# Kernel optimization log

Measured on AMD Instinct MI355X. Metric: run time of the kernel, lower is better.

The kernel has to match this reference:

```python
import jax, jax.numpy as jnp
import numpy as np
from math import sqrt

B, L, S, H, E, D = 2, 2048, 2048, 16, 64, 64

def setup_inputs() -> dict:
    key = jax.random.key(0)
    kq, kk, kv = jax.random.split(key, 3)
    queries = jax.random.normal(kq, (B, L, H, E), dtype=jnp.float32)
    keys = jax.random.normal(kk, (B, S, H, E), dtype=jnp.float32)
    values = jax.random.normal(kv, (B, S, H, D), dtype=jnp.float32)
    # causal mask: True where attention is NOT allowed (j > i), matching masked_fill_ semantics
    causal = jnp.triu(jnp.ones((L, S), dtype=jnp.bool_), k=1)
    attn_mask = jnp.broadcast_to(causal[None, None, :, :], (B, 1, L, S))
    return {"queries": queries, "keys": keys, "values": values, "attn_mask": attn_mask}

def reference(queries, keys, values, attn_mask):
    # scores: [B,H,L,S]
    scale = 1.0 / sqrt(queries.shape[-1])
    scores = jnp.einsum('blhe,bshe->bhls', queries, keys)
    scores = jnp.where(attn_mask, -jnp.inf, scores)
    A = jax.nn.softmax(scale * scores, axis=-1)
    V = jnp.einsum('bhls,bshd->blhd', A, values)
    return V
```

## Files before the change

kernel.cpp:

```cpp
#include <hip/hip_runtime.h>

typedef unsigned short ushort_t;
typedef __attribute__((ext_vector_type(8))) short s8v;
typedef __attribute__((ext_vector_type(2))) unsigned u2v;
typedef __attribute__((ext_vector_type(4))) float f4;

__device__ __forceinline__ ushort_t f2bf(float x) {
    unsigned u = __builtin_bit_cast(unsigned, x);
    return (ushort_t)((u + 0x7FFFu + ((u >> 16) & 1u)) >> 16);
}
__device__ __forceinline__ unsigned pack_hi16(float lo, float hi) {
    unsigned a = __builtin_bit_cast(unsigned, lo);
    unsigned b = __builtin_bit_cast(unsigned, hi);
    return (a >> 16) | (b & 0xFFFF0000u);
}

__global__ __launch_bounds__(256) void prep_kv(const float* __restrict__ K,
                                               const float* __restrict__ V,
                                               ushort_t* __restrict__ Kb,
                                               ushort_t* __restrict__ VT) {
    __shared__ ushort_t T[64 * 72];
    if (blockIdx.x < 2048) {
        const int gid = blockIdx.x * 256 + threadIdx.x;
        const int e = (gid & 7) * 8;
        const int h = (gid >> 3) & 15;
        const int s = (gid >> 7) & 2047;
        const int b = gid >> 18;
        const float* src = K + (((b * 2048 + s) * 16 + h) * 64 + e);
        f4 a = *(const f4*)src;
        f4 c = *(const f4*)(src + 4);
        s8v o;
        #pragma unroll
        for (int j = 0; j < 4; ++j) { o[j] = (short)f2bf(a[j]); o[j + 4] = (short)f2bf(c[j]); }
        *(s8v*)(Kb + (((b * 16 + h) * 2048 + s) * 64 + e)) = o;
    } else {
        const int v = blockIdx.x - 2048;
        const int s0 = (v & 31) * 64;
        const int h  = (v >> 5) & 15;
        const int b  = v >> 9;
        const int t  = threadIdx.x;
        {
            const int srow = t >> 2, dc = (t & 3) * 16;
            const float* src = V + (((b * 2048 + s0 + srow) * 16 + h) * 64 + dc);
            #pragma unroll
            for (int c = 0; c < 4; ++c) {
                f4 vv = *(const f4*)(src + c * 4);
                #pragma unroll
                for (int j = 0; j < 4; ++j) T[(dc + c * 4 + j) * 72 + srow] = f2bf(vv[j]);
            }
        }
        __syncthreads();
        {
            const int d = t >> 2, sq = (t & 3) * 16;
            ushort_t* dst = VT + (((b * 16 + h) * 64 + d) * 2048 + s0 + sq);
            *(s8v*)(dst)     = *(const s8v*)(&T[d * 72 + sq]);
            *(s8v*)(dst + 8) = *(const s8v*)(&T[d * 72 + sq + 8]);
        }
    }
}

__global__ __launch_bounds__(256, 2) void fattn_main(
    const float* __restrict__ Q,
    const ushort_t* __restrict__ Kb,
    const ushort_t* __restrict__ VTb,
    float* __restrict__ O)
{
    constexpr float K1 = 0.18033688011112042f;
    constexpr float SHIFT = 12.0f;
    __shared__ ushort_t KT [64 * 72];
    __shared__ ushort_t VTl[64 * 72];
    __shared__ ushort_t P  [4][16 * 72];

    const int bx = blockIdx.x;
    const int bh = bx & 31;
    const int p  = bx >> 5;
    const int b = bh >> 4, h = bh & 15;

    const int wave = threadIdx.x >> 6;
    const int lane = threadIdx.x & 63;
    const int l15  = lane & 15;
    const int quad = lane >> 4;

    const ushort_t* kb  = Kb  + bh * (2048 * 64);
    const ushort_t* vtb = VTb + bh * (64 * 2048);
    const float*    qb  = Q + b * (2048 * 1024) + h * 64;
    float*          ob  = O + b * (2048 * 1024) + h * 64;

    const s8v ones = {0x3F80, 0x3F80, 0x3F80, 0x3F80, 0x3F80, 0x3F80, 0x3F80, 0x3F80};
    const f4 zero4 = {0.f, 0.f, 0.f, 0.f};

    const int sr = threadIdx.x >> 2;
    const int sc = (threadIdx.x & 3) << 4;

    int qr0 = p * 64;

    s8v aq[2];
    f4 oacc[4];
    f4 lsum;

    auto loadQ = [&](int qr) {
        const float* qrow = qb + (qr + wave * 16 + l15) * 1024;
        #pragma unroll
        for (int ks = 0; ks < 2; ++ks) {
            f4 x = *(const f4*)(qrow + ks * 32 + quad * 8);
            f4 y = *(const f4*)(qrow + ks * 32 + quad * 8 + 4);
            #pragma unroll
            for (int j = 0; j < 4; ++j) {
                aq[ks][j]     = (short)f2bf(x[j]);
                aq[ks][j + 4] = (short)f2bf(y[j]);
            }
        }
    };
    auto zeroAcc = [&]() {
        lsum = zero4;
        #pragma unroll
        for (int d = 0; d < 4; ++d) oacc[d] = zero4;
    };
    auto storeO = [&](int qr) {
        #pragma unroll
        for (int r = 0; r < 4; ++r) {
            const float inv = 1.0f / lsum[r];
            const int row = qr + wave * 16 + quad * 4 + r;
            #pragma unroll
            for (int dd = 0; dd < 4; ++dd)
                ob[row * 1024 + dd * 16 + l15] = oacc[dd][r] * inv;
        }
    };

    loadQ(qr0);
    zeroAcc();

    s8v gK[2], gV[2];
    {
        const ushort_t* ksrc = kb + sr * 64 + sc;
        const ushort_t* vsrc = vtb + sr * 2048 + sc;
        gK[0] = *(const s8v*)(ksrc);     gK[1] = *(const s8v*)(ksrc + 8);
        gV[0] = *(const s8v*)(vsrc);     gV[1] = *(const s8v*)(vsrc + 8);
    }

    for (int n = 0; n < 33; ++n) {
        *(s8v*)&KT [sr * 72 + sc]     = gK[0];
        *(s8v*)&KT [sr * 72 + sc + 8] = gK[1];
        *(s8v*)&VTl[sr * 72 + sc]     = gV[0];
        *(s8v*)&VTl[sr * 72 + sc + 8] = gV[1];
        __syncthreads();

        s8v gK2[2], gV2[2];
        if (n < 32) {
            const int sn = (n + 1 <= p) ? (n + 1) : (n - p);
            const ushort_t* ksrc = kb + (sn * 64 + sr) * 64 + sc;
            const ushort_t* vsrc = vtb + sr * 2048 + sn * 64 + sc;
            gK2[0] = *(const s8v*)(ksrc);    gK2[1] = *(const s8v*)(ksrc + 8);
            gV2[0] = *(const s8v*)(vsrc);    gV2[1] = *(const s8v*)(vsrc + 8);
        }

        const int s_cur = (n <= p) ? n : (n - p - 1);
        const int n0 = s_cur * 64;
        const bool diag = (n == p) || (n == 32);

        f4 st[4];
        #pragma unroll
        for (int t = 0; t < 4; ++t) {
            const s8v bk0 = *(const s8v*)&KT[(t * 16 + l15) * 72 + quad * 8];
            const s8v bk1 = *(const s8v*)&KT[(t * 16 + l15) * 72 + 32 + quad * 8];
            f4 a = __builtin_amdgcn_mfma_f32_16x16x32_bf16(bk0, aq[0], zero4, 0, 0, 0);
            st[t] = __builtin_amdgcn_mfma_f32_16x16x32_bf16(bk1, aq[1], a, 0, 0, 0);
        }

        ushort_t* Pm = P[wave];
        #pragma unroll
        for (int t = 0; t < 4; ++t) {
            float pv[4];
            #pragma unroll
            for (int r = 0; r < 4; ++r) {
                float x = __builtin_fmaf(st[t][r], K1, -SHIFT);
                if (diag) {
                    const int gj = n0 + t * 16 + quad * 4 + r;
                    const int gi = qr0 + wave * 16 + l15;
                    if (gj > gi) x = -INFINITY;
                }
                pv[r] = __builtin_exp2f(x);
            }
            u2v pk;
            pk[0] = pack_hi16(pv[0], pv[1]);
            pk[1] = pack_hi16(pv[2], pv[3]);
            *(u2v*)&Pm[l15 * 72 + t * 16 + quad * 4] = pk;
        }

        #pragma unroll
        for (int ks = 0; ks < 2; ++ks) {
            s8v bvv[4];
            #pragma unroll
            for (int dd = 0; dd < 4; ++dd)
                bvv[dd] = *(const s8v*)&VTl[(dd * 16 + l15) * 72 + ks * 32 + quad * 8];
            const s8v ap = *(const s8v*)&Pm[l15 * 72 + ks * 32 + quad * 8];
            lsum = __builtin_amdgcn_mfma_f32_16x16x32_bf16(ap, ones, lsum, 0, 0, 0);
            #pragma unroll
            for (int dd = 0; dd < 4; ++dd)
                oacc[dd] = __builtin_amdgcn_mfma_f32_16x16x32_bf16(ap, bvv[dd], oacc[dd], 0, 0, 0);
        }

        __syncthreads();

        if (n < 32) {
            gK[0] = gK2[0]; gK[1] = gK2[1];
            gV[0] = gV2[0]; gV[1] = gV2[1];
        }

        if (n == p) {
            storeO(qr0);
            qr0 = (31 - p) * 64;
            loadQ(qr0);
            zeroAcc();
        }
    }

    storeO(qr0);
}

#define PSTR 72
__global__ __launch_bounds__(256) void fattn_fallback(
    const float* __restrict__ Q, const float* __restrict__ K,
    const float* __restrict__ V, float* __restrict__ O)
{
    constexpr int strL = 1024, strB = 2048 * strL;
    const float scale = 0.125f;
    __shared__ ushort_t KT[64 * PSTR];
    __shared__ ushort_t VT[64 * PSTR];
    __shared__ ushort_t P[4][16 * PSTR];
    const int bh = blockIdx.x & 31;
    const int b = bh >> 4, h = bh & 15;
    const int im = 31 - (blockIdx.x >> 5);
    const int q0 = im * 64;
    const int tid = threadIdx.x, wave = tid >> 6, lane = tid & 63;
    const int l15 = lane & 15, quad = lane >> 4;
    const float* qbase = Q + b*strB + (q0 + wave*16 + l15)*strL + h*64;
    s8v aq0, aq1;
    {
        f4 q0v = *(const f4*)(qbase + quad*8);
        f4 q1v = *(const f4*)(qbase + quad*8 + 4);
        f4 q2v = *(const f4*)(qbase + 32 + quad*8);
        f4 q3v = *(const f4*)(qbase + 32 + quad*8 + 4);
        #pragma unroll
        for (int j = 0; j < 4; ++j) {
            aq0[j] = (short)f2bf(q0v[j]); aq0[j+4] = (short)f2bf(q1v[j]);
            aq1[j] = (short)f2bf(q2v[j]); aq1[j+4] = (short)f2bf(q3v[j]);
        }
    }
    const f4 zero4 = {0.f,0.f,0.f,0.f};
    f4 oacc[4]; float m_prev[4], lsum[4];
    #pragma unroll
    for (int d = 0; d < 4; ++d) oacc[d] = zero4;
    #pragma unroll
    for (int r = 0; r < 4; ++r) { m_prev[r] = -INFINITY; lsum[r] = 0.0f; }
    const float* kh = K + b*strB + h*64;
    const float* vh = V + b*strB + h*64;
    for (int it = 0; it <= im; ++it) {
        const int n0 = it * 64;
        __syncthreads();
        {
            const float* krow = kh + (n0 + lane)*strL + wave*16;
            f4 k0 = *(const f4*)(krow); f4 k1 = *(const f4*)(krow+4);
            f4 k2 = *(const f4*)(krow+8); f4 k3 = *(const f4*)(krow+12);
            s8v kb0, kb1;
            #pragma unroll
            for (int j = 0; j < 4; ++j) {
                kb0[j] = (short)f2bf(k0[j]); kb0[j+4] = (short)f2bf(k1[j]);
                kb1[j] = (short)f2bf(k2[j]); kb1[j+4] = (short)f2bf(k3[j]);
            }
            *(s8v*)&KT[lane*PSTR + wave*16] = kb0;
            *(s8v*)&KT[lane*PSTR + wave*16 + 8] = kb1;
            const float* vrow = vh + (n0 + lane)*strL + wave*16;
            f4 v0 = *(const f4*)(vrow); f4 v1 = *(const f4*)(vrow+4);
            f4 v2 = *(const f4*)(vrow+8); f4 v3 = *(const f4*)(vrow+12);
            #pragma unroll
            for (int j = 0; j < 4; ++j) {
                VT[(wave*16 + j)*PSTR + lane] = f2bf(v0[j]);
                VT[(wave*16 + 4 + j)*PSTR + lane] = f2bf(v1[j]);
                VT[(wave*16 + 8 + j)*PSTR + lane] = f2bf(v2[j]);
                VT[(wave*16 + 12 + j)*PSTR + lane] = f2bf(v3[j]);
            }
        }
        __syncthreads();
        f4 sacc[4];
        #pragma unroll
        for (int t = 0; t < 4; ++t) {
            sacc[t] = zero4;
            const s8v bk0 = *(const s8v*)&KT[(t*16 + l15)*PSTR + quad*8];
            const s8v bk1 = *(const s8v*)&KT[(t*16 + l15)*PSTR + 32 + quad*8];
            sacc[t] = __builtin_amdgcn_mfma_f32_16x16x32_bf16(aq0, bk0, sacc[t], 0, 0, 0);
            sacc[t] = __builtin_amdgcn_mfma_f32_16x16x32_bf16(aq1, bk1, sacc[t], 0, 0, 0);
        }
        const bool diag = (it == im);
        float sv[4][4], rmax[4];
        #pragma unroll
        for (int r = 0; r < 4; ++r) rmax[r] = -INFINITY;
        #pragma unroll
        for (int t = 0; t < 4; ++t)
            #pragma unroll
            for (int r = 0; r < 4; ++r) {
                float x = sacc[t][r] * scale;
                if (diag) {
                    const int gi = wave*16 + quad*4 + r;
                    const int gj = t*16 + l15;
                    if (gj > gi) x = -INFINITY;
                }
                sv[t][r] = x; rmax[r] = fmaxf(rmax[r], x);
            }
        #pragma unroll
        for (int off = 8; off >= 1; off >>= 1)
            #pragma unroll
            for (int r = 0; r < 4; ++r)
                rmax[r] = fmaxf(rmax[r], __shfl_xor(rmax[r], off, 64));
        float mnew[4], alpha[4], rsum[4];
        #pragma unroll
        for (int r = 0; r < 4; ++r) {
            mnew[r] = fmaxf(m_prev[r], rmax[r]);
            alpha[r] = __expf(m_prev[r] - mnew[r]);
            m_prev[r] = mnew[r]; rsum[r] = 0.f;
        }
        #pragma unroll
        for (int t = 0; t < 4; ++t)
            #pragma unroll
            for (int r = 0; r < 4; ++r) {
                const float p = __expf(sv[t][r] - mnew[r]);
                rsum[r] += p;
                P[wave][(quad*4 + r)*PSTR + t*16 + l15] = f2bf(p);
            }
        #pragma unroll
        for (int off = 8; off >= 1; off >>= 1)
            #pragma unroll
            for (int r = 0; r < 4; ++r)
                rsum[r] += __shfl_xor(rsum[r], off, 64);
        #pragma unroll
        for (int r = 0; r < 4; ++r) lsum[r] = alpha[r]*lsum[r] + rsum[r];
        #pragma unroll
        for (int d = 0; d < 4; ++d)
            #pragma unroll
            for (int r = 0; r < 4; ++r) oacc[d][r] *= alpha[r];
        #pragma unroll
        for (int ks = 0; ks < 2; ++ks) {
            const s8v ap = *(const s8v*)&P[wave][l15*PSTR + ks*32 + quad*8];
            #pragma unroll
            for (int d = 0; d < 4; ++d) {
                const s8v bvv = *(const s8v*)&VT[(d*16 + l15)*PSTR + ks*32 + quad*8];
                oacc[d] = __builtin_amdgcn_mfma_f32_16x16x32_bf16(ap, bvv, oacc[d], 0, 0, 0);
            }
        }
    }
    float* obase = O + b*strB + h*64;
    #pragma unroll
    for (int r = 0; r < 4; ++r) {
        const float inv = 1.0f / lsum[r];
        const int gi = q0 + wave*16 + quad*4 + r;
        #pragma unroll
        for (int d = 0; d < 4; ++d)
            obase[gi*strL + d*16 + l15] = oacc[d][r] * inv;
    }
}

extern "C" void kernel_launch(void* const* d_in, const int* in_sizes, int n_in,
                              void* d_out, int out_size, void* d_ws, size_t ws_size,
                              hipStream_t stream) {
    const float* Q = (const float*)d_in[0];
    const float* K = (const float*)d_in[1];
    const float* V = (const float*)d_in[2];
    float* O = (float*)d_out;
    const size_t NEED = 2ull * 4194304ull * 2ull;
    if (ws_size >= NEED) {
        ushort_t* Kb = (ushort_t*)d_ws;
        ushort_t* VT = Kb + 4194304;
        prep_kv<<<3072, 256, 0, stream>>>(K, V, Kb, VT);
        fattn_main<<<512, 256, 0, stream>>>(Q, Kb, VT, O);
    } else {
        fattn_fallback<<<1024, 256, 0, stream>>>(Q, K, V, O);
    }
}
```

Baseline: 151.8 us.

## Double-buffer K/V tiles in LDS and raise wave priority around MFMA blocks

```diff
diff --git a/kernel.cpp b/kernel.cpp
--- a/kernel.cpp
+++ b/kernel.cpp
@@ -67,8 +67,10 @@
 {
     constexpr float K1 = 0.18033688011112042f;
     constexpr float SHIFT = 12.0f;
-    __shared__ ushort_t KT [64 * 72];
-    __shared__ ushort_t VTl[64 * 72];
+    __shared__ ushort_t KT0[64 * 72];
+    __shared__ ushort_t KT1[64 * 72];
+    __shared__ ushort_t VT0[64 * 72];
+    __shared__ ushort_t VT1[64 * 72];
     __shared__ ushort_t P  [4][16 * 72];
 
     const int bx = blockIdx.x;
@@ -130,21 +132,24 @@
     loadQ(qr0);
     zeroAcc();
 
-    s8v gK[2], gV[2];
     {
         const ushort_t* ksrc = kb + sr * 64 + sc;
         const ushort_t* vsrc = vtb + sr * 2048 + sc;
-        gK[0] = *(const s8v*)(ksrc);     gK[1] = *(const s8v*)(ksrc + 8);
-        gV[0] = *(const s8v*)(vsrc);     gV[1] = *(const s8v*)(vsrc + 8);
-    }
+        s8v k0 = *(const s8v*)(ksrc);
+        s8v k1 = *(const s8v*)(ksrc + 8);
+        s8v v0 = *(const s8v*)(vsrc);
+        s8v v1 = *(const s8v*)(vsrc + 8);
+        *(s8v*)&KT0[sr * 72 + sc]     = k0;
+        *(s8v*)&KT0[sr * 72 + sc + 8] = k1;
+        *(s8v*)&VT0[sr * 72 + sc]     = v0;
+        *(s8v*)&VT0[sr * 72 + sc + 8] = v1;
+    }
+    __syncthreads();
+
+    ushort_t* ktr = KT0;  ushort_t* vtr = VT0;
+    ushort_t* ktw = KT1;  ushort_t* vtw = VT1;
 
     for (int n = 0; n < 33; ++n) {
-        *(s8v*)&KT [sr * 72 + sc]     = gK[0];
-        *(s8v*)&KT [sr * 72 + sc + 8] = gK[1];
-        *(s8v*)&VTl[sr * 72 + sc]     = gV[0];
-        *(s8v*)&VTl[sr * 72 + sc + 8] = gV[1];
-        __syncthreads();
-
         s8v gK2[2], gV2[2];
         if (n < 32) {
             const int sn = (n + 1 <= p) ? (n + 1) : (n - p);
@@ -159,13 +164,15 @@
         const bool diag = (n == p) || (n == 32);
 
         f4 st[4];
+        __builtin_amdgcn_s_setprio(1);
         #pragma unroll
         for (int t = 0; t < 4; ++t) {
-            const s8v bk0 = *(const s8v*)&KT[(t * 16 + l15) * 72 + quad * 8];
-            const s8v bk1 = *(const s8v*)&KT[(t * 16 + l15) * 72 + 32 + quad * 8];
+            const s8v bk0 = *(const s8v*)&ktr[(t * 16 + l15) * 72 + quad * 8];
+            const s8v bk1 = *(const s8v*)&ktr[(t * 16 + l15) * 72 + 32 + quad * 8];
             f4 a = __builtin_amdgcn_mfma_f32_16x16x32_bf16(bk0, aq[0], zero4, 0, 0, 0);
             st[t] = __builtin_amdgcn_mfma_f32_16x16x32_bf16(bk1, aq[1], a, 0, 0, 0);
         }
+        __builtin_amdgcn_s_setprio(0);
 
         ushort_t* Pm = P[wave];
         #pragma unroll
@@ -192,20 +199,27 @@
             s8v bvv[4];
             #pragma unroll
             for (int dd = 0; dd < 4; ++dd)
-                bvv[dd] = *(const s8v*)&VTl[(dd * 16 + l15) * 72 + ks * 32 + quad * 8];
+                bvv[dd] = *(const s8v*)&vtr[(dd * 16 + l15) * 72 + ks * 32 + quad * 8];
             const s8v ap = *(const s8v*)&Pm[l15 * 72 + ks * 32 + quad * 8];
+            __builtin_amdgcn_s_setprio(1);
             lsum = __builtin_amdgcn_mfma_f32_16x16x32_bf16(ap, ones, lsum, 0, 0, 0);
             #pragma unroll
             for (int dd = 0; dd < 4; ++dd)
                 oacc[dd] = __builtin_amdgcn_mfma_f32_16x16x32_bf16(ap, bvv[dd], oacc[dd], 0, 0, 0);
+            __builtin_amdgcn_s_setprio(0);
+        }
+
+        if (n < 32) {
+            *(s8v*)&ktw[sr * 72 + sc]     = gK2[0];
+            *(s8v*)&ktw[sr * 72 + sc + 8] = gK2[1];
+            *(s8v*)&vtw[sr * 72 + sc]     = gV2[0];
+            *(s8v*)&vtw[sr * 72 + sc + 8] = gV2[1];
         }
 
         __syncthreads();
 
-        if (n < 32) {
-            gK[0] = gK2[0]; gK[1] = gK2[1];
-            gV[0] = gV2[0]; gV[1] = gV2[1];
-        }
+        { ushort_t* t0 = ktr; ktr = ktw; ktw = t0; }
+        { ushort_t* t1 = vtr; vtr = vtw; vtw = t1; }
 
         if (n == p) {
             storeO(qr0);
```

Measured after the change: 153.5 us. No clear change (+1.1%).

## Process two KV tiles per barrier with double-buffered LDS and MFMA priority hints

Applied to the files above, without the earlier changes.

```diff
diff --git a/kernel.cpp b/kernel.cpp
--- a/kernel.cpp
+++ b/kernel.cpp
@@ -67,9 +67,9 @@
 {
     constexpr float K1 = 0.18033688011112042f;
     constexpr float SHIFT = 12.0f;
-    __shared__ ushort_t KT [64 * 72];
-    __shared__ ushort_t VTl[64 * 72];
-    __shared__ ushort_t P  [4][16 * 72];
+    __shared__ ushort_t KT[2][64 * 72];
+    __shared__ ushort_t VT[2][64 * 72];
+    __shared__ ushort_t P [4][2][16 * 72];
 
     const int bx = blockIdx.x;
     const int bh = bx & 31;
@@ -127,92 +127,204 @@
         }
     };
 
-    loadQ(qr0);
-    zeroAcc();
-
-    s8v gK[2], gV[2];
-    {
-        const ushort_t* ksrc = kb + sr * 64 + sc;
-        const ushort_t* vsrc = vtb + sr * 2048 + sc;
-        gK[0] = *(const s8v*)(ksrc);     gK[1] = *(const s8v*)(ksrc + 8);
-        gV[0] = *(const s8v*)(vsrc);     gV[1] = *(const s8v*)(vsrc + 8);
-    }
-
-    for (int n = 0; n < 33; ++n) {
-        *(s8v*)&KT [sr * 72 + sc]     = gK[0];
-        *(s8v*)&KT [sr * 72 + sc + 8] = gK[1];
-        *(s8v*)&VTl[sr * 72 + sc]     = gV[0];
-        *(s8v*)&VTl[sr * 72 + sc + 8] = gV[1];
-        __syncthreads();
-
-        s8v gK2[2], gV2[2];
-        if (n < 32) {
-            const int sn = (n + 1 <= p) ? (n + 1) : (n - p);
-            const ushort_t* ksrc = kb + (sn * 64 + sr) * 64 + sc;
-            const ushort_t* vsrc = vtb + sr * 2048 + sn * 64 + sc;
-            gK2[0] = *(const s8v*)(ksrc);    gK2[1] = *(const s8v*)(ksrc + 8);
-            gV2[0] = *(const s8v*)(vsrc);    gV2[1] = *(const s8v*)(vsrc + 8);
-        }
-
-        const int s_cur = (n <= p) ? n : (n - p - 1);
-        const int n0 = s_cur * 64;
-        const bool diag = (n == p) || (n == 32);
-
+    auto computeTile = [&](int slot, int n, bool dg) {
+        const int n0 = ((n <= p) ? n : (n - p - 1)) * 64;
         f4 st[4];
-        #pragma unroll
-        for (int t = 0; t < 4; ++t) {
-            const s8v bk0 = *(const s8v*)&KT[(t * 16 + l15) * 72 + quad * 8];
-            const s8v bk1 = *(const s8v*)&KT[(t * 16 + l15) * 72 + 32 + quad * 8];
+        __builtin_amdgcn_s_setprio(1);
+        #pragma unroll
+        for (int t = 0; t < 4; ++t) {
+            const s8v bk0 = *(const s8v*)&KT[slot][(t * 16 + l15) * 72 + quad * 8];
+            const s8v bk1 = *(const s8v*)&KT[slot][(t * 16 + l15) * 72 + 32 + quad * 8];
             f4 a = __builtin_amdgcn_mfma_f32_16x16x32_bf16(bk0, aq[0], zero4, 0, 0, 0);
             st[t] = __builtin_amdgcn_mfma_f32_16x16x32_bf16(bk1, aq[1], a, 0, 0, 0);
         }
-
-        ushort_t* Pm = P[wave];
-        #pragma unroll
-        for (int t = 0; t < 4; ++t) {
-            float pv[4];
+        __builtin_amdgcn_s_setprio(0);
+        ushort_t* Pm = P[wave][slot];
+        #pragma unroll
+        for (int t = 0; t < 4; ++t) {
+            float pv4[4];
             #pragma unroll
             for (int r = 0; r < 4; ++r) {
                 float x = __builtin_fmaf(st[t][r], K1, -SHIFT);
-                if (diag) {
+                if (dg) {
                     const int gj = n0 + t * 16 + quad * 4 + r;
                     const int gi = qr0 + wave * 16 + l15;
                     if (gj > gi) x = -INFINITY;
                 }
-                pv[r] = __builtin_exp2f(x);
+                pv4[r] = __builtin_exp2f(x);
             }
             u2v pk;
-            pk[0] = pack_hi16(pv[0], pv[1]);
-            pk[1] = pack_hi16(pv[2], pv[3]);
+            pk[0] = pack_hi16(pv4[0], pv4[1]);
+            pk[1] = pack_hi16(pv4[2], pv4[3]);
             *(u2v*)&Pm[l15 * 72 + t * 16 + quad * 4] = pk;
         }
-
         #pragma unroll
         for (int ks = 0; ks < 2; ++ks) {
             s8v bvv[4];
             #pragma unroll
             for (int dd = 0; dd < 4; ++dd)
-                bvv[dd] = *(const s8v*)&VTl[(dd * 16 + l15) * 72 + ks * 32 + quad * 8];
+                bvv[dd] = *(const s8v*)&VT[slot][(dd * 16 + l15) * 72 + ks * 32 + quad * 8];
             const s8v ap = *(const s8v*)&Pm[l15 * 72 + ks * 32 + quad * 8];
+            __builtin_amdgcn_s_setprio(1);
             lsum = __builtin_amdgcn_mfma_f32_16x16x32_bf16(ap, ones, lsum, 0, 0, 0);
             #pragma unroll
             for (int dd = 0; dd < 4; ++dd)
                 oacc[dd] = __builtin_amdgcn_mfma_f32_16x16x32_bf16(ap, bvv[dd], oacc[dd], 0, 0, 0);
-        }
-
+            __builtin_amdgcn_s_setprio(0);
+        }
+    };
+
+    auto computePair = [&](int nB, bool dgB) {
+        f4 stA[4], stB[4];
+        __builtin_amdgcn_s_setprio(1);
+        #pragma unroll
+        for (int t = 0; t < 4; ++t) {
+            const s8v bk0 = *(const s8v*)&KT[0][(t * 16 + l15) * 72 + quad * 8];
+            const s8v bk1 = *(const s8v*)&KT[0][(t * 16 + l15) * 72 + 32 + quad * 8];
+            f4 a = __builtin_amdgcn_mfma_f32_16x16x32_bf16(bk0, aq[0], zero4, 0, 0, 0);
+            stA[t] = __builtin_amdgcn_mfma_f32_16x16x32_bf16(bk1, aq[1], a, 0, 0, 0);
+        }
+        #pragma unroll
+        for (int t = 0; t < 4; ++t) {
+            const s8v bk0 = *(const s8v*)&KT[1][(t * 16 + l15) * 72 + quad * 8];
+            const s8v bk1 = *(const s8v*)&KT[1][(t * 16 + l15) * 72 + 32 + quad * 8];
+            f4 a = __builtin_amdgcn_mfma_f32_16x16x32_bf16(bk0, aq[0], zero4, 0, 0, 0);
+            stB[t] = __builtin_amdgcn_mfma_f32_16x16x32_bf16(bk1, aq[1], a, 0, 0, 0);
+        }
+        __builtin_amdgcn_s_setprio(0);
+
+        ushort_t* PA = P[wave][0];
+        #pragma unroll
+        for (int t = 0; t < 4; ++t) {
+            float pv4[4];
+            #pragma unroll
+            for (int r = 0; r < 4; ++r)
+                pv4[r] = __builtin_exp2f(__builtin_fmaf(stA[t][r], K1, -SHIFT));
+            u2v pk;
+            pk[0] = pack_hi16(pv4[0], pv4[1]);
+            pk[1] = pack_hi16(pv4[2], pv4[3]);
+            *(u2v*)&PA[l15 * 72 + t * 16 + quad * 4] = pk;
+        }
+        const int n0B = ((nB <= p) ? nB : (nB - p - 1)) * 64;
+        ushort_t* PB = P[wave][1];
+        #pragma unroll
+        for (int t = 0; t < 4; ++t) {
+            float pv4[4];
+            #pragma unroll
+            for (int r = 0; r < 4; ++r) {
+                float x = __builtin_fmaf(stB[t][r], K1, -SHIFT);
+                if (dgB) {
+                    const int gj = n0B + t * 16 + quad * 4 + r;
+                    const int gi = qr0 + wave * 16 + l15;
+                    if (gj > gi) x = -INFINITY;
+                }
+                pv4[r] = __builtin_exp2f(x);
+            }
+            u2v pk;
+            pk[0] = pack_hi16(pv4[0], pv4[1]);
+            pk[1] = pack_hi16(pv4[2], pv4[3]);
+            *(u2v*)&PB[l15 * 72 + t * 16 + quad * 4] = pk;
+        }
+
+        #pragma unroll
+        for (int ks = 0; ks < 2; ++ks) {
+            s8v bvv[4];
+            #pragma unroll
+            for (int dd = 0; dd < 4; ++dd)
+                bvv[dd] = *(const s8v*)&VT[0][(dd * 16 + l15) * 72 + ks * 32 + quad * 8];
+            const s8v ap = *(const s8v*)&PA[l15 * 72 + ks * 32 + quad * 8];
+            __builtin_amdgcn_s_setprio(1);
+            lsum = __builtin_amdgcn_mfma_f32_16x16x32_bf16(ap, ones, lsum, 0, 0, 0);
+            #pragma unroll
+            for (int dd = 0; dd < 4; ++dd)
+                oacc[dd] = __builtin_amdgcn_mfma_f32_16x16x32_bf16(ap, bvv[dd], oacc[dd], 0, 0, 0);
+            __builtin_amdgcn_s_setprio(0);
+        }
+        #pragma unroll
+        for (int ks = 0; ks < 2; ++ks) {
+            s8v bvv[4];
+            #pragma unroll
+            for (int dd = 0; dd < 4; ++dd)
+                bvv[dd] = *(const s8v*)&VT[1][(dd * 16 + l15) * 72 + ks * 32 + quad * 8];
+            const s8v ap = *(const s8v*)&PB[l15 * 72 + ks * 32 + quad * 8];
+            __builtin_amdgcn_s_setprio(1);
+            lsum = __builtin_amdgcn_mfma_f32_16x16x32_bf16(ap, ones, lsum, 0, 0, 0);
+            #pragma unroll
+            for (int dd = 0; dd < 4; ++dd)
+                oacc[dd] = __builtin_amdgcn_mfma_f32_16x16x32_bf16(ap, bvv[dd], oacc[dd], 0, 0, 0);
+            __builtin_amdgcn_s_setprio(0);
+        }
+    };
+
+    loadQ(qr0);
+    zeroAcc();
+
+    s8v gKp[2][2], gVp[2][2];
+    #pragma unroll
+    for (int t2 = 0; t2 < 2; ++t2) {
+        const int n = t2;
+        const int sn = (n <= p) ? n : (n - p - 1);
+        const ushort_t* ksrc = kb + (sn * 64 + sr) * 64 + sc;
+        const ushort_t* vsrc = vtb + sr * 2048 + sn * 64 + sc;
+        gKp[t2][0] = *(const s8v*)(ksrc);    gKp[t2][1] = *(const s8v*)(ksrc + 8);
+        gVp[t2][0] = *(const s8v*)(vsrc);    gVp[t2][1] = *(const s8v*)(vsrc + 8);
+    }
+
+    for (int k = 0; k < 17; ++k) {
+        const int nA = 2 * k, nB = 2 * k + 1;
+        const bool hasB = (k < 16);
+
+        *(s8v*)&KT[0][sr * 72 + sc]     = gKp[0][0];
+        *(s8v*)&KT[0][sr * 72 + sc + 8] = gKp[0][1];
+        *(s8v*)&VT[0][sr * 72 + sc]     = gVp[0][0];
+        *(s8v*)&VT[0][sr * 72 + sc + 8] = gVp[0][1];
+        if (hasB) {
+            *(s8v*)&KT[1][sr * 72 + sc]     = gKp[1][0];
+            *(s8v*)&KT[1][sr * 72 + sc + 8] = gKp[1][1];
+            *(s8v*)&VT[1][sr * 72 + sc]     = gVp[1][0];
+            *(s8v*)&VT[1][sr * 72 + sc + 8] = gVp[1][1];
+        }
         __syncthreads();
 
-        if (n < 32) {
-            gK[0] = gK2[0]; gK[1] = gK2[1];
-            gV[0] = gV2[0]; gV[1] = gV2[1];
-        }
-
-        if (n == p) {
+        if (hasB) {
+            {
+                const int n2 = nA + 2;
+                const int sn = (n2 <= p) ? n2 : (n2 - p - 1);
+                const ushort_t* ksrc = kb + (sn * 64 + sr) * 64 + sc;
+                const ushort_t* vsrc = vtb + sr * 2048 + sn * 64 + sc;
+                gKp[0][0] = *(const s8v*)(ksrc);    gKp[0][1] = *(const s8v*)(ksrc + 8);
+                gVp[0][0] = *(const s8v*)(vsrc);    gVp[0][1] = *(const s8v*)(vsrc + 8);
+            }
+            if (nB + 2 <= 32) {
+                const int n3 = nB + 2;
+                const int sn = (n3 <= p) ? n3 : (n3 - p - 1);
+                const ushort_t* ksrc = kb + (sn * 64 + sr) * 64 + sc;
+                const ushort_t* vsrc = vtb + sr * 2048 + sn * 64 + sc;
+                gKp[1][0] = *(const s8v*)(ksrc);    gKp[1][1] = *(const s8v*)(ksrc + 8);
+                gVp[1][0] = *(const s8v*)(vsrc);    gVp[1][1] = *(const s8v*)(vsrc + 8);
+            }
+        }
+
+        if (!hasB) {
+            computeTile(0, 32, true);
+        } else if (nA == p) {
+            computeTile(0, nA, true);
             storeO(qr0);
             qr0 = (31 - p) * 64;
             loadQ(qr0);
             zeroAcc();
-        }
+            computeTile(1, nB, false);
+        } else {
+            computePair(nB, nB == p);
+            if (nB == p) {
+                storeO(qr0);
+                qr0 = (31 - p) * 64;
+                loadQ(qr0);
+                zeroAcc();
+            }
+        }
+
+        __syncthreads();
     }
 
     storeO(qr0);
```

After: 151.6 us. Within noise of the previous version (-0.1%).
